# Kernel optimization log

Measured on AMD Instinct MI355X. Metric: run time of the kernel, lower is better.

Reference implementation:

```python
import jax, jax.numpy as jnp
import numpy as np

B, R, F, H, DIM = 256, 64, 2048, 512, 512

def setup_inputs() -> dict:
    key = jax.random.key(0)
    ks = jax.random.split(key, 8)
    s = lambda n: 1.0 / np.sqrt(n)
    return {
        "features": jax.random.normal(ks[0], (B, R, F), jnp.float32),
        "prev": jax.random.normal(ks[1], (B, H), jnp.float32),
        "W_w": jax.random.normal(ks[2], (F, DIM), jnp.float32) * s(F),
        "W_b": jnp.zeros((DIM,), jnp.float32),
        "W2_w": jax.random.normal(ks[3], (H, DIM), jnp.float32) * s(H),
        "W2_b": jnp.zeros((DIM,), jnp.float32),
        "W3_w": jax.random.normal(ks[4], (DIM, 1), jnp.float32) * s(DIM),
        "W3_b": jnp.zeros((1,), jnp.float32),
    }

def reference(features, prev, W_w, W_b, W2_w, W2_b, W3_w, W3_b):
    # prev: [B,H] -> [B,1,DIM]
    p = (prev @ W2_w + W2_b)[:, None, :]
    # features: [B,R,F] -> [B,R,DIM]
    c = jnp.einsum('brf,fd->brd', features, W_w) + W_b
    c = jnp.tanh(c + p)
    score = jnp.einsum('brd,do->bro', c, W3_w) + W3_b  # [B,R,1]
    aw = jax.nn.softmax(score, axis=1)
    q = jnp.sum(aw * features, axis=1)  # [B,F]
    return q
```

## Files before the change

### kernel.cpp

```cpp
#include <hip/hip_runtime.h>
#include <hip/hip_bf16.h>


#define B_ 256
#define R_ 64
#define F_ 2048
#define H_ 512
#define DIM_ 512

typedef short bf16x8 __attribute__((ext_vector_type(8)));
typedef float f32x4 __attribute__((ext_vector_type(4)));

__device__ __forceinline__ ushort f2bf(float x) {
  __hip_bfloat16 h = __float2bfloat16(x);
  return __builtin_bit_cast(ushort, h);
}

__device__ __forceinline__ uint4 pack8(float4 x, float4 y) {
  uint4 r;
  r.x = (uint)f2bf(x.x) | ((uint)f2bf(x.y) << 16);
  r.y = (uint)f2bf(x.z) | ((uint)f2bf(x.w) << 16);
  r.z = (uint)f2bf(y.x) | ((uint)f2bf(y.y) << 16);
  r.w = (uint)f2bf(y.z) | ((uint)f2bf(y.w) << 16);
  return r;
}

__device__ __forceinline__ void gld16(const float* g, float* l) {
  __builtin_amdgcn_global_load_lds(
      (const __attribute__((address_space(1))) unsigned int*)(g),
      (__attribute__((address_space(3))) unsigned int*)(l),
      16, 0, 0);
}

__global__ void pack_w_k(const float* __restrict__ Ww, ushort* __restrict__ wpack) {
  int idx = blockIdx.x * 256 + threadIdx.x;
  float v = Ww[idx];
  int k = idx >> 9;
  int d = idx & 511;
  int kt = k >> 5, kr = k & 31;
  int g = kr >> 3, i = kr & 7;
  int ctg = d >> 4, c = d & 15;
  size_t dst = ((size_t)((kt * 32 + ctg) * 64 + g * 16 + c)) * 8 + (size_t)i;
  wpack[dst] = f2bf(v);
}

__global__ __launch_bounds__(256) void prep_p_k(const float* __restrict__ prev,
                                                const float* __restrict__ W2w,
                                                const float* __restrict__ W2b,
                                                const float* __restrict__ Wb,
                                                float* __restrict__ pprime) {
  __shared__ float lprev[8][H_];
  int bg = blockIdx.x >> 3;
  int d0 = (blockIdx.x & 7) * 64;
  int t = threadIdx.x;
  const float4* src = reinterpret_cast<const float4*>(prev + (size_t)bg * 8 * H_);
  float4* dst = reinterpret_cast<float4*>(&lprev[0][0]);
  for (int i = t; i < 8 * H_ / 4; i += 256) dst[i] = src[i];
  __syncthreads();
  int d = d0 + (t & 63);
  int bq = t >> 6;
  float a0 = 0.f, a1 = 0.f;
  #pragma unroll 8
  for (int h = 0; h < H_; ++h) {
    float wv = W2w[h * DIM_ + d];
    a0 += lprev[bq][h] * wv;
    a1 += lprev[bq + 4][h] * wv;
  }
  float bias = W2b[d] + Wb[d];
  pprime[(size_t)(bg * 8 + bq) * DIM_ + d] = a0 + bias;
  pprime[(size_t)(bg * 8 + bq + 4) * DIM_ + d] = a1 + bias;
}

__device__ __forceinline__ float fast_tanh(float x) {
  float e = __expf(2.f * x);
  return 1.f - 2.f / (e + 1.f);
}

__global__ __launch_bounds__(512, 2) void score_k(const float* __restrict__ feat,
                                                  const ushort* __restrict__ wpack,
                                                  const float* __restrict__ pprime,
                                                  const float* __restrict__ W3,
                                                  float* __restrict__ sp) {
  int bid = blockIdx.x;
  int logical = (bid & 7) * 32 + (bid >> 3);
  int rowblk = logical >> 1;
  int colblk = logical & 1;
  int t = threadIdx.x;
  int wid = t >> 6;
  int wm = wid >> 2, wn = wid & 3;
  int l = t & 63, l15 = l & 15, g = l >> 4;

  const float* featT = feat + (size_t)rowblk * 128 * F_;

  __shared__ float4 raw4[2][2048];
  __shared__ uint4 frg[2][1024];
  __shared__ float lds_part[8][R_];

  f32x4 acc[4][4];
  #pragma unroll
  for (int rt = 0; rt < 4; ++rt)
    #pragma unroll
    for (int ct = 0; ct < 4; ++ct)
      acc[rt][ct] = (f32x4){0.f, 0.f, 0.f, 0.f};

  const float* sgj[4];
  #pragma unroll
  for (int j = 0; j < 4; ++j) {
    int r_ = wid * 16 + j * 4 + g;
    int ch = l15 ^ (r_ & 15);
    sgj[j] = featT + (size_t)r_ * F_ + ch * 4;
  }

  int crow = t >> 2;
  int rm = crow & 15;
  int cq = (t & 3) * 2;

  int ctg0 = colblk * 16 + wn * 4;

#define STAGE(buf, kt) do {                                          \
    _Pragma("unroll")                                                \
    for (int j_ = 0; j_ < 4; ++j_)                                   \
      gld16(sgj[j_] + (size_t)(kt) * 64,                             \
            (float*)&raw4[buf][(wid * 16 + j_ * 4) * 16]);           \
  } while (0)

#define LOADB(dst, kt) do {                                          \
    _Pragma("unroll")                                                \
    for (int s_ = 0; s_ < 2; ++s_)                                   \
      _Pragma("unroll")                                              \
      for (int ct_ = 0; ct_ < 4; ++ct_)                              \
        dst[s_][ct_] = *reinterpret_cast<const uint4*>(              \
            wpack + ((size_t)((kt) * 2 + s_) * 32 + (ctg0 + ct_)) * 512 + (size_t)l * 8); \
  } while (0)

#define CVT(rb, fb) do {                                             \
    _Pragma("unroll")                                                \
    for (int h_ = 0; h_ < 2; ++h_) {                                 \
      int kc_ = cq + h_;                                             \
      float4 x_ = raw4[rb][crow * 16 + ((kc_ * 2) ^ rm)];            \
      float4 y_ = raw4[rb][crow * 16 + ((kc_ * 2 + 1) ^ rm)];        \
      frg[fb][kc_ * 128 + crow] = pack8(x_, y_);                     \
    }                                                                \
  } while (0)

#define MFMA_STEP(fb) do {                                           \
    _Pragma("unroll")                                                \
    for (int s_ = 0; s_ < 2; ++s_) {                                 \
      bf16x8 af_[4];                                                 \
      _Pragma("unroll")                                              \
      for (int rt_ = 0; rt_ < 4; ++rt_)                              \
        af_[rt_] = __builtin_bit_cast(bf16x8,                        \
            frg[fb][(s_ * 4 + g) * 128 + wm * 64 + rt_ * 16 + l15]); \
      _Pragma("unroll")                                              \
      for (int ct_ = 0; ct_ < 4; ++ct_) {                            \
        bf16x8 bv_ = __builtin_bit_cast(bf16x8, bc[s_][ct_]);        \
        _Pragma("unroll")                                            \
        for (int rt_ = 0; rt_ < 4; ++rt_)                            \
          acc[rt_][ct_] = __builtin_amdgcn_mfma_f32_16x16x32_bf16(   \
              af_[rt_], bv_, acc[rt_][ct_], 0, 0, 0);                \
      }                                                              \
    }                                                                \
  } while (0)

  uint4 bc[2][4], bn[2][4];
  STAGE(0, 0);
  STAGE(1, 1);
  LOADB(bc, 0);
  asm volatile("s_waitcnt vmcnt(12)" ::: "memory");
  CVT(0, 0);

  for (int kt = 0; kt < 32; ++kt) {
    if (kt < 31) LOADB(bn, kt + 1);
    if (kt < 31) {
      asm volatile("s_waitcnt vmcnt(8) lgkmcnt(0)" ::: "memory");
    } else {
      asm volatile("s_waitcnt vmcnt(0) lgkmcnt(0)" ::: "memory");
    }
    __builtin_amdgcn_s_barrier();
    asm volatile("" ::: "memory");

    if (kt < 30) STAGE(kt & 1, kt + 2);
    if (kt < 31) CVT((kt + 1) & 1, (kt + 1) & 1);
    __builtin_amdgcn_s_setprio(1);
    MFMA_STEP(kt & 1);
    __builtin_amdgcn_s_setprio(0);
    if (kt < 31) {
      #pragma unroll
      for (int s_ = 0; s_ < 2; ++s_)
        #pragma unroll
        for (int ct_ = 0; ct_ < 4; ++ct_)
          bc[s_][ct_] = bn[s_][ct_];
    }
  }

#undef STAGE
#undef LOADB
#undef CVT
#undef MFMA_STEP

  int b0 = rowblk * 2;
  float pp[4], w3v[4];
  #pragma unroll
  for (int ct = 0; ct < 4; ++ct) {
    int col = colblk * 256 + wn * 64 + ct * 16 + l15;
    pp[ct] = pprime[(b0 + wm) * DIM_ + col];
    w3v[ct] = W3[col];
  }
  #pragma unroll
  for (int rt = 0; rt < 4; ++rt) {
    #pragma unroll
    for (int j = 0; j < 4; ++j) {
      float v = fast_tanh(acc[rt][0][j] + pp[0]) * w3v[0]
              + fast_tanh(acc[rt][1][j] + pp[1]) * w3v[1]
              + fast_tanh(acc[rt][2][j] + pp[2]) * w3v[2]
              + fast_tanh(acc[rt][3][j] + pp[3]) * w3v[3];
      v += __shfl_xor(v, 1);
      v += __shfl_xor(v, 2);
      v += __shfl_xor(v, 4);
      v += __shfl_xor(v, 8);
      if (l15 == 0) lds_part[wid][rt * 16 + g * 4 + j] = v;
    }
  }
  __syncthreads();

  if (t < 128) {
    int bb = t >> 6;
    int r = t & 63;
    float s = lds_part[bb * 4 + 0][r] + lds_part[bb * 4 + 1][r]
            + lds_part[bb * 4 + 2][r] + lds_part[bb * 4 + 3][r];
    sp[((size_t)(b0 + bb) * 2 + colblk) * R_ + r] = s;
  }
}

__global__ __launch_bounds__(256) void wsum_k(const float* __restrict__ feat,
                                              const float* __restrict__ sp,
                                              float* __restrict__ out) {
  int b = blockIdx.x >> 2;
  int f0 = (blockIdx.x & 3) * 512;
  int t = threadIdx.x;
  __shared__ float lds_aw[R_];

  if (t < R_) {
    float s = sp[((size_t)b * 2 + 0) * R_ + t] + sp[((size_t)b * 2 + 1) * R_ + t];
    float m = s;
    #pragma unroll
    for (int off = 32; off >= 1; off >>= 1) m = fmaxf(m, __shfl_xor(m, off));
    float e = __expf(s - m);
    float su = e;
    #pragma unroll
    for (int off = 32; off >= 1; off >>= 1) su += __shfl_xor(su, off);
    lds_aw[t] = e / su;
  }
  __syncthreads();

  const float* fp = feat + (size_t)b * R_ * F_ + f0 + t * 2;
  float qx = 0.f, qy = 0.f;
  #pragma unroll 8
  for (int r = 0; r < R_; ++r) {
    float a = lds_aw[r];
    float2 v = *reinterpret_cast<const float2*>(fp + (size_t)r * F_);
    qx += a * v.x;
    qy += a * v.y;
  }
  *reinterpret_cast<float2*>(out + (size_t)b * F_ + f0 + t * 2) = (float2){qx, qy};
}

extern "C" void kernel_launch(void* const* d_in, const int* in_sizes, int n_in,
                              void* d_out, int out_size, void* d_ws, size_t ws_size,
                              hipStream_t stream) {
  const float* feat = (const float*)d_in[0];
  const float* prev = (const float*)d_in[1];
  const float* Ww   = (const float*)d_in[2];
  const float* Wb   = (const float*)d_in[3];
  const float* W2w  = (const float*)d_in[4];
  const float* W2b  = (const float*)d_in[5];
  const float* W3w  = (const float*)d_in[6];
  float* out = (float*)d_out;

  ushort* wpack  = (ushort*)d_ws;
  float*  pprime = (float*)((char*)d_ws + (size_t)F_ * DIM_ * 2);
  float*  sp     = (float*)((char*)d_ws + (size_t)F_ * DIM_ * 2
                                        + (size_t)B_ * DIM_ * 4);

  pack_w_k<<<(F_ * DIM_) / 256, 256, 0, stream>>>(Ww, wpack);
  prep_p_k<<<256, 256, 0, stream>>>(prev, W2w, W2b, Wb, pprime);
  score_k<<<256, 512, 0, stream>>>(feat, wpack, pprime, W3w, sp);
  wsum_k<<<B_ * 4, 256, 0, stream>>>(feat, sp, out);
}
```

Measured before the change: 113.2 us.

## Fuse score GEMM, softmax and weighted sum into one per-batch kernel

Each block now handles one batch (64 rows by all 512 columns) rather than a 128-row by 256-column tile, so scores, softmax and the weighted feature sum run in the same kernel. This drops the separate wsum kernel and the score round trip through global memory, and the second read of features may hit in cache. The cost is that every block now reads all of the packed W, doubling W traffic, and the per-block tile shape changes. Staging moves to a 3-buffer ring with a new XOR swizzle on the bf16 fragment layout.

New measurement: 103.6 us. -8.5%, faster.

```diff
diff --git a/kernel.cpp b/kernel.cpp
--- a/kernel.cpp
+++ b/kernel.cpp
@@ -76,25 +76,22 @@
   return 1.f - 2.f / (e + 1.f);
 }
 
-__global__ __launch_bounds__(512, 2) void score_k(const float* __restrict__ feat,
+__global__ __launch_bounds__(512, 2) void fused_k(const float* __restrict__ feat,
                                                   const ushort* __restrict__ wpack,
                                                   const float* __restrict__ pprime,
                                                   const float* __restrict__ W3,
-                                                  float* __restrict__ sp) {
-  int bid = blockIdx.x;
-  int logical = (bid & 7) * 32 + (bid >> 3);
-  int rowblk = logical >> 1;
-  int colblk = logical & 1;
+                                                  float* __restrict__ out) {
+  int b = blockIdx.x;
   int t = threadIdx.x;
   int wid = t >> 6;
-  int wm = wid >> 2, wn = wid & 3;
-  int l = t & 63, l15 = l & 15, g = l >> 4;
-
-  const float* featT = feat + (size_t)rowblk * 128 * F_;
-
-  __shared__ float4 raw4[2][2048];
-  __shared__ uint4 frg[2][1024];
+  int l = t & 63;
+  int l15 = l & 15, g = l >> 4;
+  const float* featB = feat + (size_t)b * R_ * F_;
+
+  __shared__ float4 raw4[3][1024];
+  __shared__ uint4 frg[2][512];
   __shared__ float lds_part[8][R_];
+  __shared__ float lds_aw[R_];
 
   f32x4 acc[4][4];
   #pragma unroll
@@ -103,72 +100,66 @@
     for (int ct = 0; ct < 4; ++ct)
       acc[rt][ct] = (f32x4){0.f, 0.f, 0.f, 0.f};
 
-  const float* sgj[4];
-  #pragma unroll
-  for (int j = 0; j < 4; ++j) {
-    int r_ = wid * 16 + j * 4 + g;
-    int ch = l15 ^ (r_ & 15);
-    sgj[j] = featT + (size_t)r_ * F_ + ch * 4;
-  }
-
-  int crow = t >> 2;
+  const float* sgj[2];
+  #pragma unroll
+  for (int j = 0; j < 2; ++j) {
+    int r_ = wid * 8 + j * 4 + g;
+    sgj[j] = featB + (size_t)r_ * F_ + (size_t)((l15 ^ (r_ & 15)) * 4);
+  }
+
+  int crow = wid * 8 + (l >> 3);
   int rm = crow & 15;
-  int cq = (t & 3) * 2;
-
-  int ctg0 = colblk * 16 + wn * 4;
-
-#define STAGE(buf, kt) do {                                          \
-    _Pragma("unroll")                                                \
-    for (int j_ = 0; j_ < 4; ++j_)                                   \
-      gld16(sgj[j_] + (size_t)(kt) * 64,                             \
-            (float*)&raw4[buf][(wid * 16 + j_ * 4) * 16]);           \
-  } while (0)
-
-#define LOADB(dst, kt) do {                                          \
-    _Pragma("unroll")                                                \
-    for (int s_ = 0; s_ < 2; ++s_)                                   \
-      _Pragma("unroll")                                              \
-      for (int ct_ = 0; ct_ < 4; ++ct_)                              \
-        dst[s_][ct_] = *reinterpret_cast<const uint4*>(              \
-            wpack + ((size_t)((kt) * 2 + s_) * 32 + (ctg0 + ct_)) * 512 + (size_t)l * 8); \
-  } while (0)
-
-#define CVT(rb, fb) do {                                             \
-    _Pragma("unroll")                                                \
-    for (int h_ = 0; h_ < 2; ++h_) {                                 \
-      int kc_ = cq + h_;                                             \
-      float4 x_ = raw4[rb][crow * 16 + ((kc_ * 2) ^ rm)];            \
-      float4 y_ = raw4[rb][crow * 16 + ((kc_ * 2 + 1) ^ rm)];        \
-      frg[fb][kc_ * 128 + crow] = pack8(x_, y_);                     \
-    }                                                                \
-  } while (0)
-
-#define MFMA_STEP(fb) do {                                           \
-    _Pragma("unroll")                                                \
-    for (int s_ = 0; s_ < 2; ++s_) {                                 \
-      bf16x8 af_[4];                                                 \
-      _Pragma("unroll")                                              \
-      for (int rt_ = 0; rt_ < 4; ++rt_)                              \
-        af_[rt_] = __builtin_bit_cast(bf16x8,                        \
-            frg[fb][(s_ * 4 + g) * 128 + wm * 64 + rt_ * 16 + l15]); \
-      _Pragma("unroll")                                              \
-      for (int ct_ = 0; ct_ < 4; ++ct_) {                            \
-        bf16x8 bv_ = __builtin_bit_cast(bf16x8, bc[s_][ct_]);        \
-        _Pragma("unroll")                                            \
-        for (int rt_ = 0; rt_ < 4; ++rt_)                            \
-          acc[rt_][ct_] = __builtin_amdgcn_mfma_f32_16x16x32_bf16(   \
-              af_[rt_], bv_, acc[rt_][ct_], 0, 0, 0);                \
-      }                                                              \
-    }                                                                \
+  int kcw = l & 7;
+  int c2 = kcw * 2;
+
+#define STAGE(buf, kt) do {                                            \
+    gld16(sgj[0] + (size_t)(kt) * 64, (float*)&raw4[buf][(wid * 8) * 16]);      \
+    gld16(sgj[1] + (size_t)(kt) * 64, (float*)&raw4[buf][(wid * 8 + 4) * 16]);  \
+  } while (0)
+
+#define LOADB(dst, kt) do {                                            \
+    _Pragma("unroll")                                                  \
+    for (int s_ = 0; s_ < 2; ++s_)                                     \
+      _Pragma("unroll")                                                \
+      for (int ct_ = 0; ct_ < 4; ++ct_)                                \
+        dst[s_][ct_] = *reinterpret_cast<const uint4*>(                \
+            wpack + ((size_t)((kt) * 2 + s_) * 32 + (wid * 4 + ct_)) * 512 + (size_t)l * 8); \
+  } while (0)
+
+#define CVT(rb, fb) do {                                               \
+    float4 x_ = raw4[rb][crow * 16 + (c2 ^ rm)];                       \
+    float4 y_ = raw4[rb][crow * 16 + ((c2 + 1) ^ rm)];                 \
+    frg[fb][kcw * 64 + (crow ^ kcw)] = pack8(x_, y_);                  \
+  } while (0)
+
+#define MFMA_STEP(fb) do {                                             \
+    _Pragma("unroll")                                                  \
+    for (int s_ = 0; s_ < 2; ++s_) {                                   \
+      bf16x8 af_[4];                                                   \
+      int kc_ = s_ * 4 + g;                                            \
+      _Pragma("unroll")                                                \
+      for (int rt_ = 0; rt_ < 4; ++rt_)                                \
+        af_[rt_] = __builtin_bit_cast(bf16x8,                          \
+            frg[fb][kc_ * 64 + ((rt_ * 16 + l15) ^ kc_)]);             \
+      _Pragma("unroll")                                                \
+      for (int ct_ = 0; ct_ < 4; ++ct_) {                              \
+        bf16x8 bv_ = __builtin_bit_cast(bf16x8, bc[s_][ct_]);          \
+        _Pragma("unroll")                                              \
+        for (int rt_ = 0; rt_ < 4; ++rt_)                              \
+          acc[rt_][ct_] = __builtin_amdgcn_mfma_f32_16x16x32_bf16(     \
+              af_[rt_], bv_, acc[rt_][ct_], 0, 0, 0);                  \
+      }                                                                \
+    }                                                                  \
   } while (0)
 
   uint4 bc[2][4], bn[2][4];
   STAGE(0, 0);
   STAGE(1, 1);
   LOADB(bc, 0);
-  asm volatile("s_waitcnt vmcnt(12)" ::: "memory");
+  asm volatile("s_waitcnt vmcnt(10)" ::: "memory");
   CVT(0, 0);
 
+  int rb_cvt = 1, rb_stage = 2;
   for (int kt = 0; kt < 32; ++kt) {
     if (kt < 31) LOADB(bn, kt + 1);
     if (kt < 31) {
@@ -179,8 +170,8 @@
     __builtin_amdgcn_s_barrier();
     asm volatile("" ::: "memory");
 
-    if (kt < 30) STAGE(kt & 1, kt + 2);
-    if (kt < 31) CVT((kt + 1) & 1, (kt + 1) & 1);
+    if (kt < 30) STAGE(rb_stage, kt + 2);
+    if (kt < 31) CVT(rb_cvt, (kt + 1) & 1);
     __builtin_amdgcn_s_setprio(1);
     MFMA_STEP(kt & 1);
     __builtin_amdgcn_s_setprio(0);
@@ -191,6 +182,8 @@
         for (int ct_ = 0; ct_ < 4; ++ct_)
           bc[s_][ct_] = bn[s_][ct_];
     }
+    rb_cvt = (rb_cvt == 2) ? 0 : rb_cvt + 1;
+    rb_stage = (rb_stage == 2) ? 0 : rb_stage + 1;
   }
 
 #undef STAGE
@@ -198,12 +191,11 @@
 #undef CVT
 #undef MFMA_STEP
 
-  int b0 = rowblk * 2;
   float pp[4], w3v[4];
   #pragma unroll
   for (int ct = 0; ct < 4; ++ct) {
-    int col = colblk * 256 + wn * 64 + ct * 16 + l15;
-    pp[ct] = pprime[(b0 + wm) * DIM_ + col];
+    int col = wid * 64 + ct * 16 + l15;
+    pp[ct] = pprime[b * DIM_ + col];
     w3v[ct] = W3[col];
   }
   #pragma unroll
@@ -223,25 +215,10 @@
   }
   __syncthreads();
 
-  if (t < 128) {
-    int bb = t >> 6;
-    int r = t & 63;
-    float s = lds_part[bb * 4 + 0][r] + lds_part[bb * 4 + 1][r]
-            + lds_part[bb * 4 + 2][r] + lds_part[bb * 4 + 3][r];
-    sp[((size_t)(b0 + bb) * 2 + colblk) * R_ + r] = s;
-  }
-}
-
-__global__ __launch_bounds__(256) void wsum_k(const float* __restrict__ feat,
-                                              const float* __restrict__ sp,
-                                              float* __restrict__ out) {
-  int b = blockIdx.x >> 2;
-  int f0 = (blockIdx.x & 3) * 512;
-  int t = threadIdx.x;
-  __shared__ float lds_aw[R_];
-
   if (t < R_) {
-    float s = sp[((size_t)b * 2 + 0) * R_ + t] + sp[((size_t)b * 2 + 1) * R_ + t];
+    float s = 0.f;
+    #pragma unroll
+    for (int w = 0; w < 8; ++w) s += lds_part[w][t];
     float m = s;
     #pragma unroll
     for (int off = 32; off >= 1; off >>= 1) m = fmaxf(m, __shfl_xor(m, off));
@@ -253,16 +230,18 @@
   }
   __syncthreads();
 
-  const float* fp = feat + (size_t)b * R_ * F_ + f0 + t * 2;
-  float qx = 0.f, qy = 0.f;
-  #pragma unroll 8
-  for (int r = 0; r < R_; ++r) {
-    float a = lds_aw[r];
-    float2 v = *reinterpret_cast<const float2*>(fp + (size_t)r * F_);
-    qx += a * v.x;
-    qy += a * v.y;
-  }
-  *reinterpret_cast<float2*>(out + (size_t)b * F_ + f0 + t * 2) = (float2){qx, qy};
+  {
+    int f0 = t * 4;
+    float4 qa = (float4){0.f, 0.f, 0.f, 0.f};
+    const float* fp = featB + f0;
+    #pragma unroll 8
+    for (int r = 0; r < R_; ++r) {
+      float a = lds_aw[r];
+      float4 v = *reinterpret_cast<const float4*>(fp + (size_t)r * F_);
+      qa.x += a * v.x; qa.y += a * v.y; qa.z += a * v.z; qa.w += a * v.w;
+    }
+    *reinterpret_cast<float4*>(out + (size_t)b * F_ + f0) = qa;
+  }
 }
 
 extern "C" void kernel_launch(void* const* d_in, const int* in_sizes, int n_in,
@@ -279,11 +258,8 @@
 
   ushort* wpack  = (ushort*)d_ws;
   float*  pprime = (float*)((char*)d_ws + (size_t)F_ * DIM_ * 2);
-  float*  sp     = (float*)((char*)d_ws + (size_t)F_ * DIM_ * 2
-                                        + (size_t)B_ * DIM_ * 4);
 
   pack_w_k<<<(F_ * DIM_) / 256, 256, 0, stream>>>(Ww, wpack);
   prep_p_k<<<256, 256, 0, stream>>>(prev, W2w, W2b, Wb, pprime);
-  score_k<<<256, 512, 0, stream>>>(feat, wpack, pprime, W3w, sp);
-  wsum_k<<<B_ * 4, 256, 0, stream>>>(feat, sp, out);
-}
+  fused_k<<<B_, 512, 0, stream>>>(feat, wpack, pprime, W3w, out);
+}
```
